# Kernel optimization log

Hardware: AMD Instinct MI355X
Metric: run time of the kernel (lower is better)

## Reference

```python
import jax, jax.numpy as jnp
import numpy as np

HEADS = 4
DIM_HEAD = 32


def setup_inputs() -> dict:
    key = jax.random.key(0)
    k1, k2, k3 = jax.random.split(key, 3)
    b, dim, h, w = 16, 256, 64, 64
    hidden = HEADS * DIM_HEAD  # 128
    x = jax.random.normal(k1, (b, dim, h, w), dtype=jnp.float32)
    # 1x1 convs are just channel matmuls; store kernels as 2D matrices.
    W_qkv = jax.random.normal(k2, (3 * hidden, dim), dtype=jnp.float32) * 0.02
    W_out = jax.random.normal(k3, (dim, hidden), dtype=jnp.float32) * 0.02
    b_out = jnp.zeros((dim,), dtype=jnp.float32)
    return {"x": x, "W_qkv": W_qkv, "W_out": W_out, "b_out": b_out}


def reference(x, W_qkv, W_out, b_out):
    b, c, h, w = x.shape
    n = h * w
    # 1x1 conv: (b, 3*hidden, h, w) -> view (b, 3, heads, dim_head, n)
    qkv = jnp.einsum('bchw,oc->bohw', x, W_qkv)
    qkv = qkv.reshape(b, 3, HEADS, DIM_HEAD, n)
    q, k, v = qkv[:, 0], qkv[:, 1], qkv[:, 2]  # each (b, heads, dim_head, n)
    k = jax.nn.softmax(k, axis=-1)
    # context: (b, heads, dim_head, dim_head)
    context = jnp.einsum('bhdn,bhen->bhde', k, v)
    # out: (b, heads, dim_head, n)
    out = jnp.einsum('bhde,bhen->bhdn', context, q)
    out = out.reshape(b, HEADS * DIM_HEAD, h, w)
    # to_out 1x1 conv with bias
    y = jnp.einsum('bchw,oc->bohw', out, W_out) + b_out[None, :, None, None]
    return y
```

## Files before the change

kernel.cpp:

```cpp
#include <hip/hip_runtime.h>

typedef __attribute__((ext_vector_type(8))) short short8;
typedef __attribute__((ext_vector_type(4))) float f32x4;
typedef unsigned short u16;
typedef unsigned int u32;


__device__ __forceinline__ u16 f2bf(float f) {
    u32 x = __float_as_uint(f);
    u32 r = (x + 0x7fffu + ((x >> 16) & 1u)) >> 16;
    return (u16)r;
}
__device__ __forceinline__ float bf2f(u16 h) {
    return __uint_as_float(((u32)h) << 16);
}

typedef __attribute__((address_space(1))) u32 as1_u32;
typedef __attribute__((address_space(3))) u32 as3_u32;
__device__ __forceinline__ void gload16(const void* g, void* l) {
    __builtin_amdgcn_global_load_lds((as1_u32*)g, (as3_u32*)l, 16, 0, 0);
}

__global__ __launch_bounds__(256) void k_transpose(const float* __restrict__ x,
                                                   u16* __restrict__ xT,
                                                   const float* __restrict__ W,
                                                   u16* __restrict__ Wb) {
    __shared__ alignas(16) u16 tile[64 * 72];
    int t = threadIdx.x;
    int n0 = blockIdx.x * 64, c0 = blockIdx.y * 64, b = blockIdx.z;

    int flat = (b * 4 + blockIdx.y) * 64 + blockIdx.x;
    if (flat < 96) {
        int idx = flat * 256 + t;
        float4 v = *reinterpret_cast<const float4*>(W + (size_t)idx * 4);
        u32 w0 = (u32)f2bf(v.x) | ((u32)f2bf(v.y) << 16);
        u32 w1 = (u32)f2bf(v.z) | ((u32)f2bf(v.w) << 16);
        uint2 o = {w0, w1};
        *reinterpret_cast<uint2*>(Wb + (size_t)idx * 4) = o;
    }

    int rr = t >> 4, nq = (t & 15) * 4;
#pragma unroll
    for (int i = 0; i < 4; i++) {
        int cl = i * 16 + rr;
        float4 v = *reinterpret_cast<const float4*>(x + ((size_t)(b * 256 + c0 + cl) * 4096 + n0 + nq));
        u32 w0 = (u32)f2bf(v.x) | ((u32)f2bf(v.y) << 16);
        u32 w1 = (u32)f2bf(v.z) | ((u32)f2bf(v.w) << 16);
        uint2 o = {w0, w1};
        *reinterpret_cast<uint2*>(&tile[cl * 72 + nq]) = o;
    }
    __syncthreads();
    int r = t >> 3, c8 = (t & 7) * 8;
#pragma unroll
    for (int i = 0; i < 2; i++) {
        int nl = i * 32 + r;
        alignas(16) u16 vals[8];
#pragma unroll
        for (int j = 0; j < 8; j++) vals[j] = tile[(c8 + j) * 72 + nl];
        *reinterpret_cast<uint4*>(xT + ((size_t)(b * 4096 + n0 + nl) * 256 + c0 + c8)) =
            *reinterpret_cast<const uint4*>(vals);
    }
}

__global__ __launch_bounds__(512, 4) void k_fused(const u16* __restrict__ xT,
                                                  const u16* __restrict__ Wb,
                                                  float* __restrict__ part,
                                                  float* __restrict__ denp) {
    __shared__ alignas(16) char smem[70656];
    u16* sA = (u16*)smem;
    u16* sB = (u16*)(smem + 32768);
    u16* Pl = (u16*)smem;
    u16* Vl = (u16*)(smem + 34816);
    float* dpart = (float*)(smem + 69632);

    int t = threadIdx.x;
    int nt = blockIdx.x, b = blockIdx.y;
    int n0 = nt * 128;
    int lane = t & 63, wv = t >> 6, l16 = lane & 15, lq = lane >> 4;
    int wr = wv >> 1, wc = wv & 1;
    int trow = t >> 3, tc8 = (t & 7) * 8;

    f32x4 acc[4][4];
#pragma unroll
    for (int i = 0; i < 4; i++)
#pragma unroll
        for (int j = 0; j < 4; j++) acc[i][j] = (f32x4){0.f, 0.f, 0.f, 0.f};

    const u16* Asrc = Wb + 128 * 256;
    const u16* Bsrc = xT + (size_t)(b * 4096 + n0) * 256;

    for (int kc = 0; kc < 4; kc++) {
        __syncthreads();
#pragma unroll
        for (int q = 0; q < 4; q++) {
            int row = q * 64 + trow;
            gload16(Asrc + (size_t)row * 256 + kc * 64 + tc8, &sA[row * 64 + tc8]);
        }
#pragma unroll
        for (int q = 0; q < 2; q++) {
            int row = q * 64 + trow;
            gload16(Bsrc + (size_t)row * 256 + kc * 64 + tc8, &sB[row * 64 + tc8]);
        }
        __syncthreads();
#pragma unroll
        for (int ks = 0; ks < 2; ks++) {
            int col = ks * 32 + lq * 8;
            short8 af[4], bfr[4];
#pragma unroll
            for (int i = 0; i < 4; i++)
                af[i] = *reinterpret_cast<const short8*>(&sA[(wr * 64 + i * 16 + l16) * 64 + col]);
#pragma unroll
            for (int j = 0; j < 4; j++)
                bfr[j] = *reinterpret_cast<const short8*>(&sB[(wc * 64 + j * 16 + l16) * 64 + col]);
#pragma unroll
            for (int i = 0; i < 4; i++)
#pragma unroll
                for (int j = 0; j < 4; j++)
                    acc[i][j] = __builtin_amdgcn_mfma_f32_16x16x32_bf16(af[i], bfr[j], acc[i][j], 0, 0, 0);
        }
    }
    __syncthreads();

    if (wr < 2) {
#pragma unroll
        for (int i = 0; i < 4; i++) {
            int rbase = wr * 64 + i * 16 + lq * 4;
            float srow[4] = {0.f, 0.f, 0.f, 0.f};
#pragma unroll
            for (int j = 0; j < 4; j++) {
                int n = wc * 64 + j * 16 + l16;
#pragma unroll
                for (int rr = 0; rr < 4; rr++) {
                    float e = __expf(acc[i][j][rr]);
                    Pl[(rbase + rr) * 136 + n] = f2bf(e);
                    srow[rr] += e;
                }
            }
#pragma unroll
            for (int rr = 0; rr < 4; rr++) {
                float s = srow[rr];
                s += __shfl_xor(s, 1, 64); s += __shfl_xor(s, 2, 64);
                s += __shfl_xor(s, 4, 64); s += __shfl_xor(s, 8, 64);
                if (l16 == 0) dpart[(rbase + rr) * 2 + wc] = s;
            }
        }
    } else {
#pragma unroll
        for (int i = 0; i < 4; i++) {
            int rbase = (wr - 2) * 64 + i * 16 + lq * 4;
#pragma unroll
            for (int j = 0; j < 4; j++) {
                int n = wc * 64 + j * 16 + l16;
#pragma unroll
                for (int rr = 0; rr < 4; rr++)
                    Vl[(rbase + rr) * 136 + n] = f2bf(acc[i][j][rr]);
            }
        }
    }
    __syncthreads();

    int h = wv >> 1, eh = wv & 1;
    f32x4 a2[2];
    a2[0] = (f32x4){0.f, 0.f, 0.f, 0.f};
    a2[1] = (f32x4){0.f, 0.f, 0.f, 0.f};
#pragma unroll
    for (int kk = 0; kk < 4; kk++) {
        int col = kk * 32 + lq * 8;
        short8 bfr = *reinterpret_cast<const short8*>(&Vl[(h * 32 + eh * 16 + l16) * 136 + col]);
#pragma unroll
        for (int i = 0; i < 2; i++) {
            short8 af = *reinterpret_cast<const short8*>(&Pl[(h * 32 + i * 16 + l16) * 136 + col]);
            a2[i] = __builtin_amdgcn_mfma_f32_16x16x32_bf16(af, bfr, a2[i], 0, 0, 0);
        }
    }
    float* pp = part + ((size_t)(b * 32 + nt) * 4 + h) * 1024;
#pragma unroll
    for (int i = 0; i < 2; i++)
#pragma unroll
        for (int rr = 0; rr < 4; rr++)
            pp[(i * 16 + lq * 4 + rr) * 32 + eh * 16 + l16] = a2[i][rr];

    if (t < 128)
        denp[((size_t)b * 128 + t) * 32 + nt] = dpart[t * 2] + dpart[t * 2 + 1];
}

__global__ __launch_bounds__(256) void k_red(const float* __restrict__ part,
                                             const float* __restrict__ denp,
                                             float* __restrict__ C) {
    __shared__ float invd[32];
    int bh = blockIdx.x;
    int b = bh >> 2, h = bh & 3;
    int t = threadIdx.x;
    if (t < 32) {
        const float* dp = denp + ((size_t)b * 128 + h * 32 + t) * 32;
        float s = 0.f;
#pragma unroll
        for (int nt = 0; nt < 32; nt++) s += dp[nt];
        invd[t] = 1.0f / s;
    }
    __syncthreads();
    int de0 = t * 4;
    float a0 = 0.f, a1 = 0.f, a2 = 0.f, a3 = 0.f;
#pragma unroll 8
    for (int nt = 0; nt < 32; nt++) {
        f32x4 v = *reinterpret_cast<const f32x4*>(part + ((size_t)(b * 32 + nt) * 4 + h) * 1024 + de0);
        a0 += v[0]; a1 += v[1]; a2 += v[2]; a3 += v[3];
    }
    float iv = invd[de0 >> 5];
    f32x4 o = {a0 * iv, a1 * iv, a2 * iv, a3 * iv};
    *reinterpret_cast<f32x4*>(C + (size_t)bh * 1024 + de0) = o;
}

__global__ __launch_bounds__(256) void k_G(const float* __restrict__ C,
                                           const float* __restrict__ Wout,
                                           const u16* __restrict__ Wb,
                                           u16* __restrict__ Gb) {
    __shared__ float Cs[4096];
    __shared__ float Us[2048];
    int b = blockIdx.x, ot = blockIdx.y, ch = blockIdx.z, t = threadIdx.x;
    int o0 = ot * 16;
#pragma unroll
    for (int q = 0; q < 16; q++) {
        int idx = q * 256 + t;
        Cs[idx] = C[(size_t)b * 4096 + idx];
    }
    __syncthreads();
#pragma unroll
    for (int q = 0; q < 8; q++) {
        int idx = q * 256 + t;
        int ol = idx >> 7, he = idx & 127;
        int h = he >> 5, e = he & 31;
        const float* wrow = Wout + (o0 + ol) * 128 + h * 32;
        const float* crow = &Cs[h * 1024 + e];
        float a = 0.f;
#pragma unroll
        for (int d = 0; d < 32; d++) a += wrow[d] * crow[d * 32];
        Us[idx] = a;
    }
    __syncthreads();
    int ol = t >> 4, c0 = ch * 128 + (t & 15) * 8;
    float acc[8];
#pragma unroll
    for (int cc = 0; cc < 8; cc++) acc[cc] = 0.f;
    const float* Ur = &Us[ol * 128];
#pragma unroll 4
    for (int he = 0; he < 128; he++) {
        float u = Ur[he];
        short8 w8 = *reinterpret_cast<const short8*>(Wb + he * 256 + c0);
#pragma unroll
        for (int e = 0; e < 8; e++)
            acc[e] += u * bf2f((u16)w8[e]);
    }
    alignas(16) u16 ob[8];
#pragma unroll
    for (int cc = 0; cc < 8; cc++) ob[cc] = f2bf(acc[cc]);
    *reinterpret_cast<uint4*>(Gb + (size_t)(b * 256 + o0 + ol) * 256 + c0) =
        *reinterpret_cast<const uint4*>(ob);
}

__global__ __launch_bounds__(512, 4) void k_y(const u16* __restrict__ Gb,
                                              const u16* __restrict__ xT,
                                              const float* __restrict__ bout,
                                              float* __restrict__ y) {
    __shared__ alignas(16) u16 sA[256 * 64];
    __shared__ alignas(16) u16 sB[128 * 64];
    int t = threadIdx.x;
    int nt = blockIdx.x, b = blockIdx.y;
    int n0 = nt * 128;
    int lane = t & 63, wv = t >> 6, l16 = lane & 15, lq = lane >> 4;
    int wr = wv >> 1, wc = wv & 1;
    int trow = t >> 3, tc8 = (t & 7) * 8;

    f32x4 acc[4][4];
#pragma unroll
    for (int i = 0; i < 4; i++)
#pragma unroll
        for (int j = 0; j < 4; j++) acc[i][j] = (f32x4){0.f, 0.f, 0.f, 0.f};

    const u16* Asrc = Gb + (size_t)b * 256 * 256;
    const u16* Bsrc = xT + (size_t)(b * 4096 + n0) * 256;

    for (int kc = 0; kc < 4; kc++) {
        __syncthreads();
#pragma unroll
        for (int q = 0; q < 4; q++) {
            int row = q * 64 + trow;
            gload16(Asrc + (size_t)row * 256 + kc * 64 + tc8, &sA[row * 64 + tc8]);
        }
#pragma unroll
        for (int q = 0; q < 2; q++) {
            int row = q * 64 + trow;
            gload16(Bsrc + (size_t)row * 256 + kc * 64 + tc8, &sB[row * 64 + tc8]);
        }
        __syncthreads();
#pragma unroll
        for (int ks = 0; ks < 2; ks++) {
            int col = ks * 32 + lq * 8;
            short8 af[4], bfr[4];
#pragma unroll
            for (int i = 0; i < 4; i++)
                af[i] = *reinterpret_cast<const short8*>(&sA[(wr * 64 + i * 16 + l16) * 64 + col]);
#pragma unroll
            for (int j = 0; j < 4; j++)
                bfr[j] = *reinterpret_cast<const short8*>(&sB[(wc * 64 + j * 16 + l16) * 64 + col]);
#pragma unroll
            for (int i = 0; i < 4; i++)
#pragma unroll
                for (int j = 0; j < 4; j++)
                    acc[i][j] = __builtin_amdgcn_mfma_f32_16x16x32_bf16(af[i], bfr[j], acc[i][j], 0, 0, 0);
        }
    }
#pragma unroll
    for (int i = 0; i < 4; i++) {
        int obase = wr * 64 + i * 16 + lq * 4;
#pragma unroll
        for (int j = 0; j < 4; j++) {
            int n = n0 + wc * 64 + j * 16 + l16;
#pragma unroll
            for (int rr = 0; rr < 4; rr++) {
                int o = obase + rr;
                y[(size_t)(b * 256 + o) * 4096 + n] = acc[i][j][rr] + bout[o];
            }
        }
    }
}

extern "C" void kernel_launch(void* const* d_in, const int* in_sizes, int n_in,
                              void* d_out, int out_size, void* d_ws, size_t ws_size,
                              hipStream_t stream) {
    const float* x    = (const float*)d_in[0];
    const float* Wqkv = (const float*)d_in[1];
    const float* Wout = (const float*)d_in[2];
    const float* bout = (const float*)d_in[3];
    float* y = (float*)d_out;

    char* ws = (char*)d_ws;
    u16*   xT   = (u16*)(ws);
    float* part = (float*)(ws + 33554432);
    float* denp = (float*)(ws + 41943040);
    float* C    = (float*)(ws + 42205184);
    u16*   Gb   = (u16*)(ws + 42467328);
    u16*   Wb   = (u16*)(ws + 44564480);

    k_transpose<<<dim3(64, 4, 16), 256, 0, stream>>>(x, xT, Wqkv, Wb);
    k_fused    <<<dim3(32, 16), 512, 0, stream>>>(xT, Wb, part, denp);
    k_red      <<<64, 256, 0, stream>>>(part, denp, C);
    k_G        <<<dim3(16, 16, 2), 256, 0, stream>>>(C, Wout, Wb, Gb);
    k_y        <<<dim3(32, 16), 512, 0, stream>>>(Gb, xT, bout, y);
}
```

Before: 171.4 us.

## Fuse partial-context reduction into G kernel and swizzle transpose LDS tile

Removes the separate k_red launch. k_G now sums the per-tile partial contexts and denominators itself and writes straight into shared memory. k_G also drops its channel-split grid dimension, so each thread computes 16 output channels instead of 8. The transpose kernel gets an XOR swizzle on its LDS tile to reduce bank conflicts on the column reads. The trade-off is that each of the 16 ot blocks per batch re-reads the full 32-tile partial array (16x redundant global reads), and the grid is halved.

Result: slower. 199.6 us (+16.4%).

```diff
diff --git a/kernel.cpp b/kernel.cpp
--- a/kernel.cpp
+++ b/kernel.cpp
@@ -47,7 +47,8 @@
         u32 w0 = (u32)f2bf(v.x) | ((u32)f2bf(v.y) << 16);
         u32 w1 = (u32)f2bf(v.z) | ((u32)f2bf(v.w) << 16);
         uint2 o = {w0, w1};
-        *reinterpret_cast<uint2*>(&tile[cl * 72 + nq]) = o;
+        int col = nq ^ (((cl >> 3) & 7) << 3);
+        *reinterpret_cast<uint2*>(&tile[cl * 72 + col]) = o;
     }
     __syncthreads();
     int r = t >> 3, c8 = (t & 7) * 8;
@@ -56,7 +57,10 @@
         int nl = i * 32 + r;
         alignas(16) u16 vals[8];
 #pragma unroll
-        for (int j = 0; j < 8; j++) vals[j] = tile[(c8 + j) * 72 + nl];
+        for (int j = 0; j < 8; j++) {
+            int row = c8 + j;
+            vals[j] = tile[row * 72 + (nl ^ (((row >> 3) & 7) << 3))];
+        }
         *reinterpret_cast<uint4*>(xT + ((size_t)(b * 4096 + n0 + nl) * 256 + c0 + c8)) =
             *reinterpret_cast<const uint4*>(vals);
     }
@@ -184,45 +188,34 @@
         denp[((size_t)b * 128 + t) * 32 + nt] = dpart[t * 2] + dpart[t * 2 + 1];
 }
 
-__global__ __launch_bounds__(256) void k_red(const float* __restrict__ part,
-                                             const float* __restrict__ denp,
-                                             float* __restrict__ C) {
-    __shared__ float invd[32];
-    int bh = blockIdx.x;
-    int b = bh >> 2, h = bh & 3;
-    int t = threadIdx.x;
-    if (t < 32) {
-        const float* dp = denp + ((size_t)b * 128 + h * 32 + t) * 32;
-        float s = 0.f;
-#pragma unroll
-        for (int nt = 0; nt < 32; nt++) s += dp[nt];
-        invd[t] = 1.0f / s;
-    }
-    __syncthreads();
-    int de0 = t * 4;
-    float a0 = 0.f, a1 = 0.f, a2 = 0.f, a3 = 0.f;
-#pragma unroll 8
-    for (int nt = 0; nt < 32; nt++) {
-        f32x4 v = *reinterpret_cast<const f32x4*>(part + ((size_t)(b * 32 + nt) * 4 + h) * 1024 + de0);
-        a0 += v[0]; a1 += v[1]; a2 += v[2]; a3 += v[3];
-    }
-    float iv = invd[de0 >> 5];
-    f32x4 o = {a0 * iv, a1 * iv, a2 * iv, a3 * iv};
-    *reinterpret_cast<f32x4*>(C + (size_t)bh * 1024 + de0) = o;
-}
-
-__global__ __launch_bounds__(256) void k_G(const float* __restrict__ C,
+__global__ __launch_bounds__(256) void k_G(const float* __restrict__ part,
+                                           const float* __restrict__ denp,
                                            const float* __restrict__ Wout,
                                            const u16* __restrict__ Wb,
                                            u16* __restrict__ Gb) {
     __shared__ float Cs[4096];
     __shared__ float Us[2048];
-    int b = blockIdx.x, ot = blockIdx.y, ch = blockIdx.z, t = threadIdx.x;
+    __shared__ float invd[128];
+    int b = blockIdx.x, ot = blockIdx.y, t = threadIdx.x;
     int o0 = ot * 16;
+
+    if (t < 128) {
+        const float* dp = denp + ((size_t)b * 128 + t) * 32;
+        float s = 0.f;
+#pragma unroll
+        for (int nt = 0; nt < 32; nt++) s += dp[nt];
+        invd[t] = 1.0f / s;
+    }
+    __syncthreads();
 #pragma unroll
     for (int q = 0; q < 16; q++) {
         int idx = q * 256 + t;
-        Cs[idx] = C[(size_t)b * 4096 + idx];
+        int h = idx >> 10, de = idx & 1023;
+        float s = 0.f;
+#pragma unroll 8
+        for (int nt = 0; nt < 32; nt++)
+            s += part[((size_t)(b * 32 + nt) * 4 + h) * 1024 + de];
+        Cs[idx] = s * invd[idx >> 5];
     }
     __syncthreads();
 #pragma unroll
@@ -238,24 +231,28 @@
         Us[idx] = a;
     }
     __syncthreads();
-    int ol = t >> 4, c0 = ch * 128 + (t & 15) * 8;
-    float acc[8];
-#pragma unroll
-    for (int cc = 0; cc < 8; cc++) acc[cc] = 0.f;
+    int ol = t >> 4, c0 = (t & 15) * 16;
+    float acc[16];
+#pragma unroll
+    for (int cc = 0; cc < 16; cc++) acc[cc] = 0.f;
     const float* Ur = &Us[ol * 128];
 #pragma unroll 4
     for (int he = 0; he < 128; he++) {
         float u = Ur[he];
-        short8 w8 = *reinterpret_cast<const short8*>(Wb + he * 256 + c0);
-#pragma unroll
-        for (int e = 0; e < 8; e++)
-            acc[e] += u * bf2f((u16)w8[e]);
-    }
-    alignas(16) u16 ob[8];
-#pragma unroll
-    for (int cc = 0; cc < 8; cc++) ob[cc] = f2bf(acc[cc]);
-    *reinterpret_cast<uint4*>(Gb + (size_t)(b * 256 + o0 + ol) * 256 + c0) =
-        *reinterpret_cast<const uint4*>(ob);
+        short8 w0 = *reinterpret_cast<const short8*>(Wb + he * 256 + c0);
+        short8 w1 = *reinterpret_cast<const short8*>(Wb + he * 256 + c0 + 8);
+#pragma unroll
+        for (int e = 0; e < 8; e++) {
+            acc[e]     += u * bf2f((u16)w0[e]);
+            acc[8 + e] += u * bf2f((u16)w1[e]);
+        }
+    }
+    alignas(16) u16 ob[16];
+#pragma unroll
+    for (int cc = 0; cc < 16; cc++) ob[cc] = f2bf(acc[cc]);
+    u16* dst = Gb + (size_t)(b * 256 + o0 + ol) * 256 + c0;
+    *reinterpret_cast<uint4*>(dst) = *reinterpret_cast<const uint4*>(ob);
+    *reinterpret_cast<uint4*>(dst + 8) = *reinterpret_cast<const uint4*>(ob + 8);
 }
 
 __global__ __launch_bounds__(512, 4) void k_y(const u16* __restrict__ Gb,
@@ -338,13 +335,11 @@
     u16*   xT   = (u16*)(ws);
     float* part = (float*)(ws + 33554432);
     float* denp = (float*)(ws + 41943040);
-    float* C    = (float*)(ws + 42205184);
-    u16*   Gb   = (u16*)(ws + 42467328);
-    u16*   Wb   = (u16*)(ws + 44564480);
+    u16*   Gb   = (u16*)(ws + 42205184);
+    u16*   Wb   = (u16*)(ws + 44302336);
 
     k_transpose<<<dim3(64, 4, 16), 256, 0, stream>>>(x, xT, Wqkv, Wb);
     k_fused    <<<dim3(32, 16), 512, 0, stream>>>(xT, Wb, part, denp);
-    k_red      <<<64, 256, 0, stream>>>(part, denp, C);
-    k_G        <<<dim3(16, 16, 2), 256, 0, stream>>>(C, Wout, Wb, Gb);
+    k_G        <<<dim3(16, 16), 256, 0, stream>>>(part, denp, Wout, Wb, Gb);
     k_y        <<<dim3(32, 16), 512, 0, stream>>>(Gb, xT, bout, y);
 }
```
